# Performance work log

Hardware: AMD Instinct MI355X
Metric: run time of the kernel (lower is better)

The kernel has to match this reference:

```python
import jax, jax.numpy as jnp
import numpy as np

B, L, E, H, ENC, V, NL = 64, 512, 128, 512, 256, 4, 2
SOS = 4


def setup_inputs() -> dict:
    key = jax.random.key(0)
    ks = jax.random.split(key, 20)
    s = 0.05
    r = lambda k, shp: (jax.random.normal(k, shp, jnp.float32) * s)
    return {
        "encoder_outputs": jax.random.normal(ks[0], (B, L, ENC), jnp.float32),
        "targets": jax.random.randint(ks[1], (B, L), 0, V),
        "encoder_mask": jnp.ones((B, L), bool),
        "teacher_forcing_ratio": 1,
        "emb": r(ks[2], (V + 2, E)),
        "Wh": r(ks[3], (H, H)),
        "Ws": r(ks[4], (H, ENC)),
        "v": r(ks[5], (1, H)),
        "Wih0": r(ks[6], (3 * H, E + ENC)),
        "Whh0": r(ks[7], (3 * H, H)),
        "bih0": r(ks[8], (3 * H,)),
        "bhh0": r(ks[9], (3 * H,)),
        "Wih1": r(ks[10], (3 * H, H)),
        "Whh1": r(ks[11], (3 * H, H)),
        "bih1": r(ks[12], (3 * H,)),
        "bhh1": r(ks[13], (3 * H,)),
        "Wout": r(ks[14], (V, H)),
        "bout": r(ks[15], (V,)),
        "Winit": r(ks[16], (H * NL, ENC)),
        "binit": r(ks[17], (H * NL,)),
    }


def gru_cell(x, h, Wih, Whh, bih, bhh):
    # PyTorch GRUCell math
    gi = x @ Wih.T + bih
    gh = h @ Whh.T + bhh
    ir, iz, inn = jnp.split(gi, 3, axis=-1)
    hr, hz, hn = jnp.split(gh, 3, axis=-1)
    rg = jax.nn.sigmoid(ir + hr)
    zg = jax.nn.sigmoid(iz + hz)
    ng = jnp.tanh(inn + rg * hn)
    return (1.0 - zg) * ng + zg * h


def reference(encoder_outputs, targets, encoder_mask, teacher_forcing_ratio,
              emb, Wh, Ws, v, Wih0, Whh0, bih0, bhh0, Wih1, Whh1, bih1, bhh1,
              Wout, bout, Winit, binit):
    # init hidden: masked mean-pool -> linear -> tanh, (NL, B, H)
    maskf = encoder_mask[..., None].astype(jnp.float32)
    pooled = (encoder_outputs * maskf).sum(1) / jnp.clip(maskf.sum(1), 1.0)
    h0 = jnp.tanh((pooled @ Winit.T + binit).reshape(B, NL, H).transpose(1, 0, 2))

    # attention keys precomputed once (same linear applied each step in torch)
    keys = jnp.einsum('ble,he->blh', encoder_outputs, Ws)  # (B, L, H)

    # teacher forcing ratio fixed at 1 -> inputs known ahead of time
    tokens = jnp.concatenate([jnp.full((B, 1), SOS, targets.dtype), targets[:, :-1]], axis=1)
    emb_seq = emb[tokens]  # (B, L, E)

    neg = jnp.finfo(jnp.float32).min

    def step(h, e_t):
        q = h[-1] @ Wh.T                                   # (B, H)
        energy = jnp.tanh(q[:, None, :] + keys)            # (B, L, H)
        scores = jnp.einsum('blh,h->bl', energy, v[0])     # (B, L)
        scores = jnp.where(encoder_mask, scores, neg)
        attn = jax.nn.softmax(scores, axis=-1)
        ctx = jnp.einsum('bl,ble->be', attn, encoder_outputs)
        x = jnp.concatenate([e_t, ctx], axis=-1)           # (B, E+ENC)
        h0n = gru_cell(x, h[0], Wih0, Whh0, bih0, bhh0)
        h1n = gru_cell(h0n, h[1], Wih1, Whh1, bih1, bhh1)
        logits = h1n @ Wout.T + bout                       # (B, V)
        return jnp.stack([h0n, h1n]), logits

    _, logits = jax.lax.scan(step, h0, emb_seq.transpose(1, 0, 2))
    return logits.transpose(1, 0, 2)  # (B, L, V)
```

## Files before the change

kernel.cpp:

```cpp
#include <hip/hip_runtime.h>
#include <cstdint>
#include <cstddef>


#define BB   64
#define LL   512
#define EE   128
#define HH   512
#define ED   256
#define VV   4
#define SOS  4

#define NBLK 512
#define NTHR 256

typedef unsigned short ushort8 __attribute__((ext_vector_type(8)));
typedef unsigned int uint;

static const size_t OFF_KEYS = 0;
static const size_t OFF_WH   = 33554432;
static const size_t OFF_WHH0 = 34078720;
static const size_t OFF_WIH1 = 35651584;
static const size_t OFF_WHH1 = 37224448;
static const size_t OFF_WIHC = 38797312;
static const size_t OFF_GTOK = 39583744;
static const size_t OFF_H0   = 39620608;
static const size_t OFF_H1   = 39751680;
static const size_t OFF_QQ   = 39882752;
static const size_t OFF_CTXP = 40407040;
static const size_t OFF_SS   = 40931328;
static const size_t OFF_H0Q  = 40933376;
static const size_t OFF_H1Q  = 40998912;
static const size_t OFF_FLG  = 41064448;
static const size_t OFF_CNT  = 41097216;
static const size_t OFF_LP   = 41097728;

#define L_KEYS 0
#define L_H0F  65536
#define L_H1F  66560
#define L_QB   67584
#define L_VV   69696
#define L_CTX  71808
#define L_SCB  72832
#define L_ATB  73088
#define L_RED  73344
#define L_PRED 73408
#define L_GH0  76480
#define L_GH1  77248
#define L_H0O  78016
#define L_H1O  78272
#define L_TOT  78528

__device__ __forceinline__ float bfu(unsigned short u) {
  return __uint_as_float(((unsigned)u) << 16);
}
__device__ __forceinline__ float bflo(uint u) { return __uint_as_float(u << 16); }
__device__ __forceinline__ float bfhi(uint u) { return __uint_as_float(u & 0xffff0000u); }
__device__ __forceinline__ unsigned short f2bf(float f) {
  unsigned u = __float_as_uint(f);
  unsigned r = 0x7FFFu + ((u >> 16) & 1u);
  return (unsigned short)((u + r) >> 16);
}
__device__ __forceinline__ uint packbf(float a, float b) {
  return (uint)f2bf(a) | ((uint)f2bf(b) << 16);
}
__device__ __forceinline__ float tanh_fast(float x) {
  x = __builtin_amdgcn_fmed3f(x, -10.f, 10.f);
  float t = __builtin_amdgcn_exp2f(x * 2.8853900817779268f);
  return (t - 1.f) * __builtin_amdgcn_rcpf(t + 1.f);
}
__device__ __forceinline__ float sigmoid_fast(float x) {
  x = __builtin_amdgcn_fmed3f(x, -30.f, 30.f);
  float t = __builtin_amdgcn_exp2f(x * -1.4426950408889634f);
  return __builtin_amdgcn_rcpf(1.f + t);
}
__device__ __forceinline__ float exp_fast(float x) {
  return __builtin_amdgcn_exp2f(x * 1.4426950408889634f);
}
__device__ __forceinline__ float gloadf(const float* p) {
  return __hip_atomic_load(p, __ATOMIC_RELAXED, __HIP_MEMORY_SCOPE_AGENT);
}
__device__ __forceinline__ void gstoref(float* p, float v) {
  __hip_atomic_store(p, v, __ATOMIC_RELAXED, __HIP_MEMORY_SCOPE_AGENT);
}
__device__ __forceinline__ uint gloadu(const uint* p) {
  return __hip_atomic_load(p, __ATOMIC_RELAXED, __HIP_MEMORY_SCOPE_AGENT);
}
__device__ __forceinline__ void gstoreu(uint* p, uint v) {
  __hip_atomic_store(p, v, __ATOMIC_RELAXED, __HIP_MEMORY_SCOPE_AGENT);
}

__device__ __forceinline__ void octet_sync(char* ws, int b, int j, uint gen) {
  asm volatile("s_waitcnt vmcnt(0)" ::: "memory");
  __syncthreads();
  const int tid = threadIdx.x;
  uint* fl = (uint*)(ws + OFF_FLG);
  if (tid == 0)
    gstoreu(fl + (size_t)(b * 8 + j) * 16, gen);
  if (tid < 8 && tid != j) {
    while (gloadu(fl + (size_t)(b * 8 + tid) * 16) < gen)
      __builtin_amdgcn_s_sleep(4);
  }
  __syncthreads();
}


__global__ void k_prep(const float* Wh, const float* Whh0, const float* Wih0,
                       const float* Wih1, const float* Whh1, char* ws) {
  unsigned short* Whbf   = (unsigned short*)(ws + OFF_WH);
  unsigned short* Whh0bf = (unsigned short*)(ws + OFF_WHH0);
  unsigned short* Wih1bf = (unsigned short*)(ws + OFF_WIH1);
  unsigned short* Whh1bf = (unsigned short*)(ws + OFF_WHH1);
  unsigned short* WihCbf = (unsigned short*)(ws + OFF_WIHC);
  const int tot = 262144 + 786432 * 3 + 393216;
  for (int i = blockIdx.x * blockDim.x + threadIdx.x; i < tot; i += gridDim.x * blockDim.x) {
    if (i < 262144) { Whbf[i] = f2bf(Wh[i]); }
    else if (i < 262144 + 786432) { int jj = i - 262144; Whh0bf[jj] = f2bf(Whh0[jj]); }
    else if (i < 262144 + 2 * 786432) { int jj = i - 262144 - 786432; Wih1bf[jj] = f2bf(Wih1[jj]); }
    else if (i < 262144 + 3 * 786432) { int jj = i - 262144 - 2 * 786432; Whh1bf[jj] = f2bf(Whh1[jj]); }
    else {
      int jj = i - 262144 - 3 * 786432;
      int r = jj >> 8, e = jj & 255;
      WihCbf[jj] = f2bf(Wih0[(size_t)r * 384 + 128 + e]);
    }
  }
}

__global__ void k_gitok(const float* emb, const float* Wih0, const float* bih0, char* ws) {
  float* gt = (float*)(ws + OFF_GTOK);
  const int vt = blockIdx.x;
  const int tid = threadIdx.x;
  __shared__ float ev[EE];
  if (tid < EE) ev[tid] = emb[(size_t)vt * EE + tid];
  __syncthreads();
  for (int r = tid; r < 1536; r += 256) {
    float a = bih0[r];
    const float* wr = Wih0 + (size_t)r * 384;
    for (int e = 0; e < EE; ++e) a += wr[e] * ev[e];
    gt[(size_t)vt * 1536 + r] = a;
  }
}

__global__ void k_keys(const float* enc, const float* Ws, char* ws) {
  unsigned short* keys = (unsigned short*)(ws + OFF_KEYS);
  __shared__ float et[32][ED];
  const int tid = threadIdx.x;
  const int row0 = blockIdx.x * 32;
  for (int r = 0; r < 32; ++r) et[r][tid] = enc[(size_t)(row0 + r) * ED + tid];
  __syncthreads();
  for (int hhh = 0; hhh < 2; ++hhh) {
    const int h = hhh * 256 + tid;
    float acc[32];
    #pragma unroll
    for (int ll = 0; ll < 32; ++ll) acc[ll] = 0.f;
    const float4* wrow = (const float4*)(Ws + (size_t)h * ED);
    for (int e4 = 0; e4 < 64; ++e4) {
      float4 w = wrow[e4];
      #pragma unroll
      for (int ll = 0; ll < 32; ++ll) {
        acc[ll] += w.x * et[ll][e4 * 4] + w.y * et[ll][e4 * 4 + 1]
                 + w.z * et[ll][e4 * 4 + 2] + w.w * et[ll][e4 * 4 + 3];
      }
    }
    for (int ll = 0; ll < 32; ++ll)
      keys[(size_t)(row0 + ll) * HH + h] = f2bf(acc[ll]);
  }
}

__global__ void k_init(const float* enc, const float* Winit, const float* binit, char* ws) {
  const int b = blockIdx.x;
  const int tid = threadIdx.x;
  __shared__ float pooled[ED];
  float acc = 0.f;
  for (int l = 0; l < LL; ++l) acc += enc[((size_t)b * LL + l) * ED + tid];
  pooled[tid] = acc * (1.0f / 512.0f);
  __syncthreads();
  float* h0 = (float*)(ws + OFF_H0);
  float* h1 = (float*)(ws + OFF_H1);
  for (int pass = 0; pass < 4; ++pass) {
    const int jj = pass * 256 + tid;
    float a = binit[jj];
    const float* wr = Winit + (size_t)jj * ED;
    for (int e = 0; e < ED; ++e) a += wr[e] * pooled[e];
    const float val = tanh_fast(a);
    const int nl = jj >> 9, h = jj & 511;
    if (nl == 0) h0[(size_t)b * HH + h] = val;
    else h1[(size_t)b * HH + h] = val;
  }
  if (b == 0) {
    uint* fl = (uint*)(ws + OFF_FLG);
    for (int i = tid; i < 8192; i += 256) fl[i] = 0u;
    uint* cnt = (uint*)(ws + OFF_CNT);
    if (tid < 128) cnt[tid] = 0u;
  }
}

__launch_bounds__(NTHR, 2)
__global__ void k_decode(char* ws, const float* enc, const int* targets,
                         const float* vvec, const float* bhh0, const float* bhh1,
                         const float* bih1, const float* Wout) {
  extern __shared__ char smem[];
  const int tid = threadIdx.x;

  __shared__ int roleSh[2];
  if (tid == 0) {
    uint xcd;
    asm volatile("s_getreg_b32 %0, hwreg(HW_REG_XCC_ID)" : "=s"(xcd));
    xcd &= 7u;
    uint* cnt = (uint*)(ws + OFF_CNT);
    uint rank = __hip_atomic_fetch_add(cnt + (size_t)xcd * 16, 1u,
                                       __ATOMIC_RELAXED, __HIP_MEMORY_SCOPE_AGENT);
    roleSh[0] = (int)(rank & 63);
    roleSh[1] = (int)xcd;
  }
  __syncthreads();
  const int b = roleSh[0], j = roleSh[1];

  const unsigned short* keysg  = (const unsigned short*)(ws + OFF_KEYS);
  const unsigned short* Whbf   = (const unsigned short*)(ws + OFF_WH);
  const unsigned short* Whh0bf = (const unsigned short*)(ws + OFF_WHH0);
  const unsigned short* Wih1bf = (const unsigned short*)(ws + OFF_WIH1);
  const unsigned short* Whh1bf = (const unsigned short*)(ws + OFF_WHH1);
  const unsigned short* WihCbf = (const unsigned short*)(ws + OFF_WIHC);
  const float* gi_tok = (const float*)(ws + OFF_GTOK);

  uint*  QQg   = (uint*)(ws + OFF_QQ)   + (size_t)b * 2048;
  float* CTXPg = (float*)(ws + OFF_CTXP) + (size_t)b * 2048;
  float* SSg   = (float*)(ws + OFF_SS)  + (size_t)b * 8;
  uint*  H0Qg  = (uint*)(ws + OFF_H0Q)  + (size_t)b * 256;
  uint*  H1Qg  = (uint*)(ws + OFF_H1Q)  + (size_t)b * 256;
  float* lp    = (float*)(ws + OFF_LP);

  uint*  h0u   = (uint*)(smem + L_H0F);
  uint*  h1u   = (uint*)(smem + L_H1F);
  float* qbf   = (float*)(smem + L_QB);
  float* vvf   = (float*)(smem + L_VV);
  float* ctx   = (float*)(smem + L_CTX);
  float* scb   = (float*)(smem + L_SCB);
  float* atb   = (float*)(smem + L_ATB);
  float* wred  = (float*)(smem + L_RED);
  float* pRed  = (float*)(smem + L_PRED);
  float* gh0own = (float*)(smem + L_GH0);
  float* gh1own = (float*)(smem + L_GH1);
  float* h0own = (float*)(smem + L_H0O);
  float* h1own = (float*)(smem + L_H1O);

  for (int c = tid; c < 4096; c += NTHR) {
    const int l = c >> 6, hs = c & 63;
    ushort8 kv = *(const ushort8*)(keysg + ((size_t)(b * LL + j * 64 + l) * HH + hs * 8));
    *(ushort8*)(smem + L_KEYS + l * 1024 + ((hs * 16) ^ ((l & 7) << 4))) = kv;
  }
  for (int h = tid; h < 512; h += NTHR)
    vvf[(h >> 7) * 132 + (h & 127)] = vvec[h];
  {
    const float* H0g = (const float*)(ws + OFF_H0) + (size_t)b * HH;
    const float* H1g = (const float*)(ws + OFF_H1) + (size_t)b * HH;
    h0u[tid] = packbf(H0g[2 * tid], H0g[2 * tid + 1]);
    h1u[tid] = packbf(H1g[2 * tid], H1g[2 * tid + 1]);
    if (tid < 64) {
      h0own[tid] = H0g[j * 64 + tid];
      h1own[tid] = H1g[j * 64 + tid];
    }
  }
  uint encp[32];
  {
    const float* ebase = enc + ((size_t)(b * LL + j * 64)) * ED + tid;
    #pragma unroll
    for (int k = 0; k < 32; ++k)
      encp[k] = packbf(ebase[(size_t)(2 * k) * ED], ebase[(size_t)(2 * k + 1) * ED]);
  }
  uint whq[64];
  #pragma unroll
  for (int i = 0; i < 32; ++i) {
    whq[i]      = *(const uint*)(Whbf + (size_t)(2 * tid) * HH + j * 64 + 2 * i);
    whq[32 + i] = *(const uint*)(Whbf + (size_t)(2 * tid + 1) * HH + j * 64 + 2 * i);
  }
  __syncthreads();

  {
    float q0 = 0.f, q1 = 0.f;
    #pragma unroll
    for (int i = 0; i < 32; ++i) {
      const float hl = h1own[2 * i], hh = h1own[2 * i + 1];
      q0 += bflo(whq[i]) * hl + bfhi(whq[i]) * hh;
      q1 += bflo(whq[32 + i]) * hl + bfhi(whq[32 + i]) * hh;
    }
    gstoreu(QQg + (size_t)j * 256 + tid, packbf(q0, q1));
    if (tid < 32) gstoreu(H1Qg + (size_t)j * 32 + tid,
                          packbf(h1own[2 * tid], h1own[2 * tid + 1]));
  }
  octet_sync(ws, b, j, 1u);

  for (int t = 0; t < LL; ++t) {
    {
      float qlo = 0.f, qhi = 0.f;
      #pragma unroll
      for (int p = 0; p < 8; ++p) {
        uint u = gloadu(QQg + (size_t)p * 256 + tid);
        qlo += bflo(u); qhi += bfhi(u);
      }
      const int hq = tid >> 6, i2 = (tid & 63) * 2;
      qbf[hq * 132 + i2] = qlo;
      qbf[hq * 132 + i2 + 1] = qhi;
      if (tid < 224) {
        const int ps = tid >> 5, i = tid & 31;
        const int p = ps + (ps >= j);
        h1u[p * 32 + i] = gloadu(H1Qg + (size_t)p * 32 + i);
      }
    }
    __syncthreads();

    {
      const int mat = tid >> 7, seg = (tid >> 6) & 1, r = tid & 63;
      const unsigned short* W = mat ? Whh1bf : Whh0bf;
      const uint* hsrc = (mat ? h1u : h0u) + seg * 128;
      const ushort8* w0 = (const ushort8*)(W + (size_t)(0 * 512 + j * 64 + r) * 512 + seg * 256);
      const ushort8* w1 = (const ushort8*)(W + (size_t)(1 * 512 + j * 64 + r) * 512 + seg * 256);
      const ushort8* w2 = (const ushort8*)(W + (size_t)(2 * 512 + j * 64 + r) * 512 + seg * 256);
      float a0 = 0.f, a1 = 0.f, a2 = 0.f;
      for (int k8 = 0; k8 < 32; ++k8) {
        const uint4 hu = *(const uint4*)(hsrc + k8 * 4);
        const ushort8 u0 = w0[k8], u1 = w1[k8], u2 = w2[k8];
        float hv[8];
        hv[0] = bflo(hu.x); hv[1] = bfhi(hu.x); hv[2] = bflo(hu.y); hv[3] = bfhi(hu.y);
        hv[4] = bflo(hu.z); hv[5] = bfhi(hu.z); hv[6] = bflo(hu.w); hv[7] = bfhi(hu.w);
        #pragma unroll
        for (int u = 0; u < 8; ++u) {
          a0 += bfu(u0[u]) * hv[u];
          a1 += bfu(u1[u]) * hv[u];
          a2 += bfu(u2[u]) * hv[u];
        }
      }
      pRed[((mat * 2 + seg) * 3 + 0) * 64 + r] = a0;
      pRed[((mat * 2 + seg) * 3 + 1) * 64 + r] = a1;
      pRed[((mat * 2 + seg) * 3 + 2) * 64 + r] = a2;
    }

    {
      const int lloc = tid >> 2, hq = tid & 3;
      const char* kbase = smem + L_KEYS + lloc * 1024;
      const int xo = (lloc & 7) << 4;
      const float* qh = qbf + hq * 132;
      const float* vh = vvf + hq * 132;
      float s = 0.f;
      for (int i8 = 0; i8 < 16; ++i8) {
        ushort8 kk = *(const ushort8*)(kbase + ((hq * 256 + i8 * 16) ^ xo));
        const float* q8 = qh + i8 * 8;
        const float* v8 = vh + i8 * 8;
        #pragma unroll
        for (int u = 0; u < 8; ++u)
          s += v8[u] * tanh_fast(q8[u] + bfu(kk[u]));
      }
      s += __shfl_xor(s, 1);
      s += __shfl_xor(s, 2);
      if (hq == 0) scb[lloc] = s;
    }
    __syncthreads();

    if (tid < 64) {
      float e = exp_fast(scb[tid]);
      atb[tid] = e;
      float s2 = e;
      #pragma unroll
      for (int off = 32; off >= 1; off >>= 1) s2 += __shfl_xor(s2, off);
      if (tid == 0) gstoref(SSg + j, s2);
    }
    __syncthreads();

    {
      float a = 0.f;
      #pragma unroll
      for (int k = 0; k < 32; ++k) {
        uint u = encp[k];
        a += atb[2 * k] * bflo(u) + atb[2 * k + 1] * bfhi(u);
      }
      gstoref(CTXPg + (size_t)j * 256 + tid, a);
    }
    for (int o = tid; o < 384; o += NTHR) {
      const int m = (o >= 192) ? 1 : 0, oo = o - m * 192, g = oo >> 6, r = oo & 63;
      const float v = pRed[((m * 2 + 0) * 3 + g) * 64 + r]
                    + pRed[((m * 2 + 1) * 3 + g) * 64 + r]
                    + (m ? bhh1 : bhh0)[g * 512 + j * 64 + r];
      (m ? gh1own : gh0own)[g * 64 + r] = v;
    }
    octet_sync(ws, b, j, (uint)(3 * t + 2));

    {
      float cp0 = gloadf(CTXPg + 0 * 256 + tid), cp1 = gloadf(CTXPg + 1 * 256 + tid);
      float cp2 = gloadf(CTXPg + 2 * 256 + tid), cp3 = gloadf(CTXPg + 3 * 256 + tid);
      float cp4 = gloadf(CTXPg + 4 * 256 + tid), cp5 = gloadf(CTXPg + 5 * 256 + tid);
      float cp6 = gloadf(CTXPg + 6 * 256 + tid), cp7 = gloadf(CTXPg + 7 * 256 + tid);
      if (tid < 8) wred[tid] = gloadf(SSg + tid);
      __syncthreads();
      const float S8 = ((wred[0] + wred[1]) + (wred[2] + wred[3]))
                     + ((wred[4] + wred[5]) + (wred[6] + wred[7]));
      const float rS = __builtin_amdgcn_rcpf(S8);
      ctx[tid] = (((cp0 + cp1) + (cp2 + cp3)) + ((cp4 + cp5) + (cp6 + cp7))) * rS;
    }
    __syncthreads();
    {
      const int r = tid & 63, q4 = tid >> 6;
      const ushort8* w0 = (const ushort8*)(WihCbf + (size_t)(0 * 512 + j * 64 + r) * 256 + q4 * 64);
      const ushort8* w1 = (const ushort8*)(WihCbf + (size_t)(1 * 512 + j * 64 + r) * 256 + q4 * 64);
      const ushort8* w2 = (const ushort8*)(WihCbf + (size_t)(2 * 512 + j * 64 + r) * 256 + q4 * 64);
      const float* cx = ctx + q4 * 64;
      float a0 = 0.f, a1 = 0.f, a2 = 0.f;
      for (int k8 = 0; k8 < 8; ++k8) {
        const ushort8 u0 = w0[k8], u1 = w1[k8], u2 = w2[k8];
        #pragma unroll
        for (int u = 0; u < 8; ++u) {
          const float c = cx[k8 * 8 + u];
          a0 += bfu(u0[u]) * c; a1 += bfu(u1[u]) * c; a2 += bfu(u2[u]) * c;
        }
      }
      pRed[(q4 * 3 + 0) * 64 + r] = a0;
      pRed[(q4 * 3 + 1) * 64 + r] = a1;
      pRed[(q4 * 3 + 2) * 64 + r] = a2;
    }
    __syncthreads();
    if (tid < 64) {
      const int r = tid;
      const int tok = (t == 0) ? SOS : targets[(size_t)b * LL + t - 1];
      const float* gt = gi_tok + (size_t)tok * 1536 + j * 64 + r;
      const float g0 = pRed[(0 * 3 + 0) * 64 + r] + pRed[(1 * 3 + 0) * 64 + r]
                     + pRed[(2 * 3 + 0) * 64 + r] + pRed[(3 * 3 + 0) * 64 + r] + gt[0];
      const float g1 = pRed[(0 * 3 + 1) * 64 + r] + pRed[(1 * 3 + 1) * 64 + r]
                     + pRed[(2 * 3 + 1) * 64 + r] + pRed[(3 * 3 + 1) * 64 + r] + gt[512];
      const float g2 = pRed[(0 * 3 + 2) * 64 + r] + pRed[(1 * 3 + 2) * 64 + r]
                     + pRed[(2 * 3 + 2) * 64 + r] + pRed[(3 * 3 + 2) * 64 + r] + gt[1024];
      const float rg = sigmoid_fast(g0 + gh0own[r]);
      const float zg = sigmoid_fast(g1 + gh0own[64 + r]);
      const float ng = tanh_fast(g2 + rg * gh0own[128 + r]);
      h0own[r] = (1.f - zg) * ng + zg * h0own[r];
    }
    __syncthreads();
    if (tid < 32) {
      const uint pk = packbf(h0own[2 * tid], h0own[2 * tid + 1]);
      h0u[j * 32 + tid] = pk;
      gstoreu(H0Qg + (size_t)j * 32 + tid, pk);
    }
    octet_sync(ws, b, j, (uint)(3 * t + 3));

    if (tid < 224) {
      const int ps = tid >> 5, i = tid & 31;
      const int p = ps + (ps >= j);
      h0u[p * 32 + i] = gloadu(H0Qg + (size_t)p * 32 + i);
    }
    __syncthreads();
    {
      const int r = tid & 63, s4 = tid >> 6;
      const ushort8* w0 = (const ushort8*)(Wih1bf + (size_t)(0 * 512 + j * 64 + r) * 512 + s4 * 128);
      const ushort8* w1 = (const ushort8*)(Wih1bf + (size_t)(1 * 512 + j * 64 + r) * 512 + s4 * 128);
      const ushort8* w2 = (const ushort8*)(Wih1bf + (size_t)(2 * 512 + j * 64 + r) * 512 + s4 * 128);
      const uint* hsrc = h0u + s4 * 64;
      float a0 = 0.f, a1 = 0.f, a2 = 0.f;
      for (int k8 = 0; k8 < 16; ++k8) {
        const uint4 hu = *(const uint4*)(hsrc + k8 * 4);
        const ushort8 u0 = w0[k8], u1 = w1[k8], u2 = w2[k8];
        float hv[8];
        hv[0] = bflo(hu.x); hv[1] = bfhi(hu.x); hv[2] = bflo(hu.y); hv[3] = bfhi(hu.y);
        hv[4] = bflo(hu.z); hv[5] = bfhi(hu.z); hv[6] = bflo(hu.w); hv[7] = bfhi(hu.w);
        #pragma unroll
        for (int u = 0; u < 8; ++u) {
          a0 += bfu(u0[u]) * hv[u];
          a1 += bfu(u1[u]) * hv[u];
          a2 += bfu(u2[u]) * hv[u];
        }
      }
      pRed[(s4 * 3 + 0) * 64 + r] = a0;
      pRed[(s4 * 3 + 1) * 64 + r] = a1;
      pRed[(s4 * 3 + 2) * 64 + r] = a2;
    }
    __syncthreads();
    if (tid < 64) {
      const int r = tid;
      const float g0 = pRed[(0 * 3 + 0) * 64 + r] + pRed[(1 * 3 + 0) * 64 + r]
                     + pRed[(2 * 3 + 0) * 64 + r] + pRed[(3 * 3 + 0) * 64 + r]
                     + bih1[0 * 512 + j * 64 + r];
      const float g1 = pRed[(0 * 3 + 1) * 64 + r] + pRed[(1 * 3 + 1) * 64 + r]
                     + pRed[(2 * 3 + 1) * 64 + r] + pRed[(3 * 3 + 1) * 64 + r]
                     + bih1[1 * 512 + j * 64 + r];
      const float g2 = pRed[(0 * 3 + 2) * 64 + r] + pRed[(1 * 3 + 2) * 64 + r]
                     + pRed[(2 * 3 + 2) * 64 + r] + pRed[(3 * 3 + 2) * 64 + r]
                     + bih1[2 * 512 + j * 64 + r];
      const float rg = sigmoid_fast(g0 + gh1own[r]);
      const float zg = sigmoid_fast(g1 + gh1own[64 + r]);
      const float ng = tanh_fast(g2 + rg * gh1own[128 + r]);
      h1own[r] = (1.f - zg) * ng + zg * h1own[r];
    }
    __syncthreads();
    if (tid < 32) {
      const uint pk = packbf(h1own[2 * tid], h1own[2 * tid + 1]);
      h1u[j * 32 + tid] = pk;
      gstoreu(H1Qg + (size_t)j * 32 + tid, pk);
    }
    {
      float q0 = 0.f, q1 = 0.f;
      #pragma unroll
      for (int i = 0; i < 32; ++i) {
        const float hl = h1own[2 * i], hh = h1own[2 * i + 1];
        q0 += bflo(whq[i]) * hl + bfhi(whq[i]) * hh;
        q1 += bflo(whq[32 + i]) * hl + bfhi(whq[32 + i]) * hh;
      }
      gstoreu(QQg + (size_t)j * 256 + tid, packbf(q0, q1));
    }
    if (tid >= 64 && tid < 128) {
      const int lane = tid - 64, v = lane >> 4, i = lane & 15;
      float a = 0.f;
      #pragma unroll
      for (int k = 0; k < 4; ++k)
        a += Wout[(size_t)v * HH + j * 64 + i * 4 + k] * h1own[i * 4 + k];
      a += __shfl_xor(a, 8); a += __shfl_xor(a, 4);
      a += __shfl_xor(a, 2); a += __shfl_xor(a, 1);
      if (i == 0) lp[(((size_t)t * BB + b) * 8 + j) * 4 + v] = a;
    }
    octet_sync(ws, b, j, (uint)(3 * t + 4));
  }
}

__global__ void k_lsum(const char* ws, const float* bout, float* out) {
  const float* lp = (const float*)(ws + OFF_LP);
  const int i = blockIdx.x * 256 + threadIdx.x;
  if (i >= BB * LL * VV) return;
  const int v = i & 3, t = (i >> 2) & 511, b = i >> 11;
  float a = bout[v];
  #pragma unroll
  for (int jj = 0; jj < 8; ++jj)
    a += lp[(((size_t)t * BB + b) * 8 + jj) * 4 + v];
  out[i] = a;
}

extern "C" void kernel_launch(void* const* d_in, const int* in_sizes, int n_in,
                              void* d_out, int out_size, void* d_ws, size_t ws_size,
                              hipStream_t stream) {
  char* ws = (char*)d_ws;
  const float* enc     = (const float*)d_in[0];
  const int*   targets = (const int*)d_in[1];
  const float* emb   = (const float*)d_in[4];
  const float* Wh    = (const float*)d_in[5];
  const float* Ws    = (const float*)d_in[6];
  const float* vvec  = (const float*)d_in[7];
  const float* Wih0  = (const float*)d_in[8];
  const float* Whh0  = (const float*)d_in[9];
  const float* bih0  = (const float*)d_in[10];
  const float* bhh0  = (const float*)d_in[11];
  const float* Wih1  = (const float*)d_in[12];
  const float* Whh1  = (const float*)d_in[13];
  const float* bih1  = (const float*)d_in[14];
  const float* bhh1  = (const float*)d_in[15];
  const float* Wout  = (const float*)d_in[16];
  const float* bout  = (const float*)d_in[17];
  const float* Winit = (const float*)d_in[18];
  const float* binit = (const float*)d_in[19];

  k_prep <<<1024, 256, 0, stream>>>(Wh, Whh0, Wih0, Wih1, Whh1, ws);
  k_gitok<<<6,    256, 0, stream>>>(emb, Wih0, bih0, ws);
  k_keys <<<1024, 256, 0, stream>>>(enc, Ws, ws);
  k_init <<<64,   256, 0, stream>>>(enc, Winit, binit, ws);

  (void)hipFuncSetAttribute((const void*)k_decode,
                            hipFuncAttributeMaxDynamicSharedMemorySize, L_TOT);

  {
    void* kws = (void*)ws;
    void* ken = (void*)enc;
    void* ktg = (void*)targets;
    void* kvv = (void*)vvec;
    void* kb0 = (void*)bhh0;
    void* kb1 = (void*)bhh1;
    void* kbi = (void*)bih1;
    void* kwo = (void*)Wout;
    void* args[] = { &kws, &ken, &ktg, &kvv, &kb0, &kb1, &kbi, &kwo };
    hipError_t ce = hipLaunchCooperativeKernel((const void*)k_decode, dim3(NBLK), dim3(NTHR),
                                               args, L_TOT, stream);
    if (ce != hipSuccess) {
      k_decode<<<dim3(NBLK), dim3(NTHR), L_TOT, stream>>>(ws, enc, targets, vvec,
                                                          bhh0, bhh1, bih1, Wout);
    }
  }

  k_lsum<<<512, 256, 0, stream>>>(ws, bout, (float*)d_out);
}
```

Baseline: 49.90 ms.

## Vectorize cross-block exchange with uncached dwordx4 loads/stores via LDS staging

Per-step exchanges of q, h0, h1 and context partials between the 8 cooperating blocks now stage values in shared memory and move them with 16-byte uncached global loads and stores (sc0 sc1) issued by a few threads. Before, all threads did scalar accesses. The context partial reduction is split into two halves, combined in shared memory. The goal is fewer global memory transactions and less latency on the serial inter-block sync path, at the cost of extra __syncthreads and a larger shared-memory layout.

```diff
diff --git a/kernel.cpp b/kernel.cpp
--- a/kernel.cpp
+++ b/kernel.cpp
@@ -16,6 +16,8 @@
 
 typedef unsigned short ushort8 __attribute__((ext_vector_type(8)));
 typedef unsigned int uint;
+typedef uint  uint4v  __attribute__((ext_vector_type(4)));
+typedef float float4v __attribute__((ext_vector_type(4)));
 
 static const size_t OFF_KEYS = 0;
 static const size_t OFF_WH   = 33554432;
@@ -45,11 +47,19 @@
 #define L_ATB  73088
 #define L_RED  73344
 #define L_PRED 73408
-#define L_GH0  76480
-#define L_GH1  77248
-#define L_H0O  78016
-#define L_H1O  78272
-#define L_TOT  78528
+#define L_GH0  77504
+#define L_GH1  78272
+#define L_H0O  79040
+#define L_H1O  79296
+#define L_TOT  79552
+
+#define UC_LD4(dst, ptr) \
+  asm volatile("global_load_dwordx4 %0, %1, off sc0 sc1" : "=v"(dst) : "v"(ptr))
+#define UC_ST4(ptr, v4) \
+  asm volatile("global_store_dwordx4 %0, %1, off sc0 sc1" :: "v"(ptr), "v"(v4) : "memory")
+#define UC_FENCE() \
+  do { asm volatile("s_waitcnt vmcnt(0)" ::: "memory"); \
+       __builtin_amdgcn_sched_barrier(0); } while (0)
 
 __device__ __forceinline__ float bfu(unsigned short u) {
   return __uint_as_float(((unsigned)u) << 16);
@@ -244,6 +254,8 @@
   float* gh1own = (float*)(smem + L_GH1);
   float* h0own = (float*)(smem + L_H0O);
   float* h1own = (float*)(smem + L_H1O);
+  uint*  qstage = (uint*)(smem + L_PRED);
+  uint*  hstage = (uint*)(smem + L_SCB);
 
   for (int c = tid; c < 4096; c += NTHR) {
     const int l = c >> 6, hs = c & 63;
@@ -285,28 +297,46 @@
       q0 += bflo(whq[i]) * hl + bfhi(whq[i]) * hh;
       q1 += bflo(whq[32 + i]) * hl + bfhi(whq[32 + i]) * hh;
     }
-    gstoreu(QQg + (size_t)j * 256 + tid, packbf(q0, q1));
-    if (tid < 32) gstoreu(H1Qg + (size_t)j * 32 + tid,
-                          packbf(h1own[2 * tid], h1own[2 * tid + 1]));
+    qstage[tid] = packbf(q0, q1);
+    if (tid < 32) hstage[tid] = packbf(h1own[2 * tid], h1own[2 * tid + 1]);
+    __syncthreads();
+    if (tid < 64) { UC_ST4(QQg + (size_t)j * 256 + 4 * tid, *(uint4v*)(qstage + 4 * tid)); }
+    else if (tid < 72) {
+      const int c = tid - 64;
+      UC_ST4(H1Qg + (size_t)j * 32 + 4 * c, *(uint4v*)(hstage + 4 * c));
+    }
   }
   octet_sync(ws, b, j, 1u);
 
   for (int t = 0; t < LL; ++t) {
-    {
-      float qlo = 0.f, qhi = 0.f;
+    if (tid < 64) {
+      uint4v uq0, uq1, uq2, uq3, uq4, uq5, uq6, uq7;
+      UC_LD4(uq0, QQg + 0 * 256 + 4 * tid);
+      UC_LD4(uq1, QQg + 1 * 256 + 4 * tid);
+      UC_LD4(uq2, QQg + 2 * 256 + 4 * tid);
+      UC_LD4(uq3, QQg + 3 * 256 + 4 * tid);
+      UC_LD4(uq4, QQg + 4 * 256 + 4 * tid);
+      UC_LD4(uq5, QQg + 5 * 256 + 4 * tid);
+      UC_LD4(uq6, QQg + 6 * 256 + 4 * tid);
+      UC_LD4(uq7, QQg + 7 * 256 + 4 * tid);
+      UC_FENCE();
+      const int base = ((8 * tid) >> 7) * 132 + ((8 * tid) & 127);
       #pragma unroll
-      for (int p = 0; p < 8; ++p) {
-        uint u = gloadu(QQg + (size_t)p * 256 + tid);
-        qlo += bflo(u); qhi += bfhi(u);
-      }
-      const int hq = tid >> 6, i2 = (tid & 63) * 2;
-      qbf[hq * 132 + i2] = qlo;
-      qbf[hq * 132 + i2 + 1] = qhi;
-      if (tid < 224) {
-        const int ps = tid >> 5, i = tid & 31;
-        const int p = ps + (ps >= j);
-        h1u[p * 32 + i] = gloadu(H1Qg + (size_t)p * 32 + i);
-      }
+      for (int k = 0; k < 4; ++k) {
+        float lo = bflo(uq0[k]) + bflo(uq1[k]) + bflo(uq2[k]) + bflo(uq3[k])
+                 + bflo(uq4[k]) + bflo(uq5[k]) + bflo(uq6[k]) + bflo(uq7[k]);
+        float hi = bfhi(uq0[k]) + bfhi(uq1[k]) + bfhi(uq2[k]) + bfhi(uq3[k])
+                 + bfhi(uq4[k]) + bfhi(uq5[k]) + bfhi(uq6[k]) + bfhi(uq7[k]);
+        qbf[base + 2 * k]     = lo;
+        qbf[base + 2 * k + 1] = hi;
+      }
+    } else if (tid < 120) {
+      const int p2 = (tid - 64) >> 3, c = (tid - 64) & 7;
+      const int p = p2 + (p2 >= j);
+      uint4v u;
+      UC_LD4(u, H1Qg + (size_t)p * 32 + 4 * c);
+      UC_FENCE();
+      *(uint4v*)(h1u + p * 32 + 4 * c) = u;
     }
     __syncthreads();
 
@@ -374,7 +404,7 @@
         uint u = encp[k];
         a += atb[2 * k] * bflo(u) + atb[2 * k + 1] * bfhi(u);
       }
-      gstoref(CTXPg + (size_t)j * 256 + tid, a);
+      ctx[tid] = a;
     }
     for (int o = tid; o < 384; o += NTHR) {
       const int m = (o >= 192) ? 1 : 0, oo = o - m * 192, g = oo >> 6, r = oo & 63;
@@ -383,19 +413,26 @@
                     + (m ? bhh1 : bhh0)[g * 512 + j * 64 + r];
       (m ? gh1own : gh0own)[g * 64 + r] = v;
     }
+    __syncthreads();
+    if (tid < 64) { UC_ST4((uint*)(CTXPg + (size_t)j * 256) + 4 * tid, *(uint4v*)((uint*)ctx + 4 * tid)); }
     octet_sync(ws, b, j, (uint)(3 * t + 2));
 
     {
-      float cp0 = gloadf(CTXPg + 0 * 256 + tid), cp1 = gloadf(CTXPg + 1 * 256 + tid);
-      float cp2 = gloadf(CTXPg + 2 * 256 + tid), cp3 = gloadf(CTXPg + 3 * 256 + tid);
-      float cp4 = gloadf(CTXPg + 4 * 256 + tid), cp5 = gloadf(CTXPg + 5 * 256 + tid);
-      float cp6 = gloadf(CTXPg + 6 * 256 + tid), cp7 = gloadf(CTXPg + 7 * 256 + tid);
-      if (tid < 8) wred[tid] = gloadf(SSg + tid);
+      const int c = tid & 63, p0 = tid >> 6;
+      float4v f0, f1;
+      UC_LD4(f0, (const uint*)(CTXPg + (size_t)p0 * 256) + 4 * c);
+      UC_LD4(f1, (const uint*)(CTXPg + (size_t)(p0 + 4) * 256) + 4 * c);
+      float ssv = 0.f;
+      if (tid < 8) ssv = gloadf(SSg + tid);
+      UC_FENCE();
+      if (tid < 8) wred[tid] = ssv;
+      *(float4v*)(pRed + (size_t)p0 * 256 + 4 * c) = f0 + f1;
       __syncthreads();
       const float S8 = ((wred[0] + wred[1]) + (wred[2] + wred[3]))
                      + ((wred[4] + wred[5]) + (wred[6] + wred[7]));
       const float rS = __builtin_amdgcn_rcpf(S8);
-      ctx[tid] = (((cp0 + cp1) + (cp2 + cp3)) + ((cp4 + cp5) + (cp6 + cp7))) * rS;
+      ctx[tid] = (pRed[0 * 256 + tid] + pRed[1 * 256 + tid]
+                + pRed[2 * 256 + tid] + pRed[3 * 256 + tid]) * rS;
     }
     __syncthreads();
     {
@@ -437,14 +474,19 @@
     if (tid < 32) {
       const uint pk = packbf(h0own[2 * tid], h0own[2 * tid + 1]);
       h0u[j * 32 + tid] = pk;
-      gstoreu(H0Qg + (size_t)j * 32 + tid, pk);
-    }
+      hstage[tid] = pk;
+    }
+    __syncthreads();
+    if (tid < 8) { UC_ST4(H0Qg + (size_t)j * 32 + 4 * tid, *(uint4v*)(hstage + 4 * tid)); }
     octet_sync(ws, b, j, (uint)(3 * t + 3));
 
-    if (tid < 224) {
-      const int ps = tid >> 5, i = tid & 31;
-      const int p = ps + (ps >= j);
-      h0u[p * 32 + i] = gloadu(H0Qg + (size_t)p * 32 + i);
+    if (tid < 56) {
+      const int p2 = tid >> 3, c = tid & 7;
+      const int p = p2 + (p2 >= j);
+      uint4v u;
+      UC_LD4(u, H0Qg + (size_t)p * 32 + 4 * c);
+      UC_FENCE();
+      *(uint4v*)(h0u + p * 32 + 4 * c) = u;
     }
     __syncthreads();
     {
@@ -489,11 +531,6 @@
       h1own[r] = (1.f - zg) * ng + zg * h1own[r];
     }
     __syncthreads();
-    if (tid < 32) {
-      const uint pk = packbf(h1own[2 * tid], h1own[2 * tid + 1]);
-      h1u[j * 32 + tid] = pk;
-      gstoreu(H1Qg + (size_t)j * 32 + tid, pk);
-    }
     {
       float q0 = 0.f, q1 = 0.f;
       #pragma unroll
@@ -502,7 +539,12 @@
         q0 += bflo(whq[i]) * hl + bfhi(whq[i]) * hh;
         q1 += bflo(whq[32 + i]) * hl + bfhi(whq[32 + i]) * hh;
       }
-      gstoreu(QQg + (size_t)j * 256 + tid, packbf(q0, q1));
+      qstage[tid] = packbf(q0, q1);
+    }
+    if (tid < 32) {
+      const uint pk = packbf(h1own[2 * tid], h1own[2 * tid + 1]);
+      h1u[j * 32 + tid] = pk;
+      hstage[tid] = pk;
     }
     if (tid >= 64 && tid < 128) {
       const int lane = tid - 64, v = lane >> 4, i = lane & 15;
@@ -513,6 +555,12 @@
       a += __shfl_xor(a, 8); a += __shfl_xor(a, 4);
       a += __shfl_xor(a, 2); a += __shfl_xor(a, 1);
       if (i == 0) lp[(((size_t)t * BB + b) * 8 + j) * 4 + v] = a;
+    }
+    __syncthreads();
+    if (tid < 64) { UC_ST4(QQg + (size_t)j * 256 + 4 * tid, *(uint4v*)(qstage + 4 * tid)); }
+    else if (tid < 72) {
+      const int c = tid - 64;
+      UC_ST4(H1Qg + (size_t)j * 32 + 4 * c, *(uint4v*)(hstage + 4 * c));
     }
     octet_sync(ws, b, j, (uint)(3 * t + 4));
   }
```

After: 49.45 ms. About the same (-0.9%).
